# Performance work log

Measured on AMD Instinct MI355X. Metric: run time of the kernel, lower is better.

## Reference

```python
import jax, jax.numpy as jnp
import numpy as np

V, E, CIN, COUT, NH, HID = 8192, 2048, 128, 128, 4, 32
EPS = 1e-5

def _ln(x, g, b):
    m = x.mean(-1, keepdims=True)
    v = x.var(-1, keepdims=True)
    return (x - m) / jnp.sqrt(v + EPS) * g + b

def setup_inputs() -> dict:
    key = jax.random.key(0)
    ks = jax.random.split(key, 12)
    s = 0.05
    X = jax.random.normal(ks[0], (V, CIN), jnp.float32)
    H = jax.random.bernoulli(ks[1], 0.02, (V, E)).astype(jnp.float32)
    edge_features = jax.random.normal(ks[2], (E, COUT), jnp.float32)
    Wv = jax.random.normal(ks[3], (CIN, COUT), jnp.float32) * s
    bv = jnp.zeros((COUT,), jnp.float32)
    We = jax.random.normal(ks[4], (COUT, COUT), jnp.float32) * s
    be = jnp.zeros((COUT,), jnp.float32)
    vW1 = jax.random.normal(ks[5], (NH, CIN, HID), jnp.float32) * s
    vb1 = jnp.zeros((NH, HID), jnp.float32)
    vW2 = jax.random.normal(ks[6], (NH, HID), jnp.float32) * s
    vb2 = jnp.zeros((NH,), jnp.float32)
    eW1 = jax.random.normal(ks[7], (COUT, HID), jnp.float32) * s
    eb1 = jnp.zeros((HID,), jnp.float32)
    eW2 = jax.random.normal(ks[8], (HID,), jnp.float32) * s
    eb2 = jnp.zeros((), jnp.float32)
    Wc = jax.random.normal(ks[9], (NH * COUT, COUT), jnp.float32) * s
    bc = jnp.zeros((COUT,), jnp.float32)
    Wg = jax.random.normal(ks[10], (CIN + COUT, COUT), jnp.float32) * s
    bg = jnp.zeros((COUT,), jnp.float32)
    return dict(X=X, H=H, edge_features=edge_features, Wv=Wv, bv=bv, We=We, be=be,
                vW1=vW1, vb1=vb1, vW2=vW2, vb2=vb2, eW1=eW1, eb1=eb1, eW2=eW2, eb2=eb2,
                Wc=Wc, bc=bc,
                ln_e_g=jnp.ones((COUT,), jnp.float32), ln_e_b=jnp.zeros((COUT,), jnp.float32),
                ln_v_g=jnp.ones((COUT,), jnp.float32), ln_v_b=jnp.zeros((COUT,), jnp.float32),
                bn_g=jnp.ones((COUT,), jnp.float32), bn_b=jnp.zeros((COUT,), jnp.float32),
                Wg=Wg, bg=bg)

def reference(X, H, edge_features, Wv, bv, We, be, vW1, vb1, vW2, vb2,
              eW1, eb1, eW2, eb2, Wc, bc, ln_e_g, ln_e_b, ln_v_g, ln_v_b,
              bn_g, bn_b, Wg, bg):
    gelu = lambda t: jax.nn.gelu(t, approximate=False)  # torch nn.GELU default (erf)
    Ht = H.T                                   # (E, V)
    Xt = X @ Wv + bv                           # (V, Cout) theta_v
    # per-head vertex attention MLP: Linear(Cin,32)->GELU->Linear(32,1), vectorized over heads
    hid = gelu(jnp.einsum('vc,hck->hvk', X, vW1) + vb1[:, None, :])
    attn = jax.nn.sigmoid(jnp.einsum('hvk,hk->hv', hid, vW2) + vb2[:, None])  # (NH, V)
    deg = Ht.sum(axis=1, keepdims=True)        # (E, 1) edge degrees
    denom = jnp.maximum(deg, 1.0)
    # degree-normalized attention-weighted v2e aggregation per head
    head_e = jnp.einsum('ev,hvc->hec', Ht, Xt[None] * attn[:, :, None]) / denom[None]
    e_cat = jnp.transpose(head_e, (1, 0, 2)).reshape(E, NH * COUT)  # concat heads dim=1
    e_feat = e_cat @ Wc + bc                   # attn_combine
    # edge attention uses the LAST head's vertex weights (global-var quirk in torch code)
    edge_att = ((Ht @ attn[-1]) / jnp.maximum(deg[:, 0], 1.0))[:, None]  # (E,1)
    # edge-feature gating with e_attention head 0
    te = edge_features @ We + be               # theta_e
    e_scores = gelu(e_feat @ eW1 + eb1) @ eW2 + eb2
    ew = jax.nn.sigmoid(e_scores)[:, None]
    e_feat = e_feat * ew + te * (1.0 - ew)
    # normalize == 'both': layer_norm_e then batch_norm (training-mode batch stats)
    e_feat = _ln(e_feat, ln_e_g, ln_e_b)
    m = e_feat.mean(axis=0)
    v = e_feat.var(axis=0)
    e_feat = (e_feat - m) / jnp.sqrt(v + EPS) * bn_g + bn_b
    # e2v sum aggregation: H @ e_feat
    v_feat = H @ e_feat                        # (V, Cout)
    gate = jax.nn.sigmoid(jnp.concatenate([X, v_feat], axis=1) @ Wg + bg)
    v_feat = gate * v_feat + (1.0 - gate) * Xt
    v_feat = _ln(v_feat, ln_v_g, ln_v_b)
    v_feat = v_feat + X                        # residual (Cin == Cout)
    v_feat = gelu(v_feat)                      # not is_last: activation; dropout = identity (eval)
    e_feat = gelu(e_feat)
    return v_feat, e_feat, edge_att
```

## Files before the change

kernel.cpp:

```cpp
#include <hip/hip_runtime.h>
#include <hip/hip_bf16.h>
#include <math.h>

#define NV 8192
#define NE 2048
#define CIN 128
#define COUT 128
#define NH 4
#define HID 32
#define EPB 4
#define LCAP 256
#define VCAP 96
#define NWORDS (NE / 64)
#define TWORDS (NV / 64)
#define EPSV 1e-5f

__device__ __forceinline__ float gelu_f(float x) {
    return 0.5f * x * (1.0f + erff(x * 0.70710678118654752f));
}
__device__ __forceinline__ float sigmoid_f(float x) {
    return 1.0f / (1.0f + expf(-x));
}

__global__ __launch_bounds__(256) void k_front(
    const float* __restrict__ X, const float* __restrict__ Wv, const float* __restrict__ bv,
    const float* __restrict__ vW1, const float* __restrict__ vb1,
    const float* __restrict__ vW2, const float* __restrict__ vb2,
    const float* __restrict__ H,
    float* __restrict__ Xt, float* __restrict__ attn4,
    unsigned long long* __restrict__ Hbits, int* __restrict__ vdeg, int* __restrict__ vlist)
{
    __shared__ float Xs[2][8][CIN];
    int t = threadIdx.x;
    if (blockIdx.x < NV / 16) {
        int half = t >> 7, tt = t & 127;
        int v0 = blockIdx.x * 16 + half * 8;
        for (int v = 0; v < 8; ++v) Xs[half][v][tt] = X[(size_t)(v0 + v) * CIN + tt];
        __syncthreads();

        float acc[8];
        float bvc = bv[tt];
#pragma unroll
        for (int v = 0; v < 8; ++v) acc[v] = bvc;
        for (int k = 0; k < CIN; ++k) {
            float w = Wv[k * COUT + tt];
#pragma unroll
            for (int v = 0; v < 8; ++v) acc[v] = fmaf(Xs[half][v][k], w, acc[v]);
        }
        for (int v = 0; v < 8; ++v) Xt[(size_t)(v0 + v) * COUT + tt] = acc[v];

        int h = tt >> 5, j = tt & 31;
        float hb = vb1[h * HID + j];
#pragma unroll
        for (int v = 0; v < 8; ++v) acc[v] = hb;
        for (int k = 0; k < CIN; ++k) {
            float w = vW1[(h * CIN + k) * HID + j];
#pragma unroll
            for (int v = 0; v < 8; ++v) acc[v] = fmaf(Xs[half][v][k], w, acc[v]);
        }
        float w2 = vW2[h * HID + j];
        float b2 = vb2[h];
        for (int v = 0; v < 8; ++v) {
            float val = gelu_f(acc[v]) * w2;
#pragma unroll
            for (int m = 16; m >= 1; m >>= 1) val += __shfl_xor(val, m, 64);
            if (j == 0) attn4[(size_t)(v0 + v) * NH + h] = sigmoid_f(val + b2);
        }
    } else {
        int b = blockIdx.x - NV / 16;
        int w = t >> 6;
        int lane = t & 63;
        int v = b * 4 + w;
        const float* row = H + (size_t)v * NE;
        unsigned long long lt = (1ull << lane) - 1ull;
        int base = 0;
        int* vl = vlist + (size_t)v * VCAP;
#pragma unroll 8
        for (int it = 0; it < NWORDS; ++it) {
            float hv = row[it * 64 + lane];
            bool nz = hv != 0.0f;
            unsigned long long m = __ballot(nz);
            if (lane == 0) Hbits[(size_t)v * NWORDS + it] = m;
            if (nz) {
                int pos = base + __popcll(m & lt);
                if (pos < VCAP) vl[pos] = it * 64 + lane;
            }
            base += __popcll(m);
        }
        if (lane == 0) vdeg[v] = base;
    }
}

__global__ __launch_bounds__(256) void k_transpose(
    const unsigned long long* __restrict__ Hbits, unsigned long long* __restrict__ HbitsT)
{
    __shared__ unsigned long long rows[64][NWORDS];
    int t = threadIdx.x;
    int vt = blockIdx.x;
    for (int i = t; i < 64 * NWORDS; i += 256)
        rows[i >> 5][i & 31] = Hbits[(size_t)vt * 64 * NWORDS + i];
    __syncthreads();
    int wv = t >> 6;
    int lane = t & 63;
    const unsigned long long M[6] = {
        0xFFFFFFFF00000000ULL, 0xFFFF0000FFFF0000ULL, 0xFF00FF00FF00FF00ULL,
        0xF0F0F0F0F0F0F0F0ULL, 0xCCCCCCCCCCCCCCCCULL, 0xAAAAAAAAAAAAAAAAULL };
    const int js[6] = {32, 16, 8, 4, 2, 1};
#pragma unroll
    for (int itb = 0; itb < 8; ++itb) {
        int it = wv * 8 + itb;
        unsigned long long x = rows[lane][it];
#pragma unroll
        for (int s = 0; s < 6; ++s) {
            int j = js[s];
            unsigned long long y = __shfl_xor(x, j, 64);
            unsigned long long Ms = M[s];
            if ((lane & j) == 0) x = (x & ~Ms) | ((y << j) & Ms);
            else                 x = (x & Ms) | ((y >> j) & ~Ms);
        }
        HbitsT[(size_t)(it * 64 + lane) * TWORDS + vt] = x;
    }
}

__global__ __launch_bounds__(512) void k_edge(
    const float* __restrict__ Xt, const float* __restrict__ attn4,
    const unsigned long long* __restrict__ HbitsT,
    const float* __restrict__ edge_features,
    const float* __restrict__ Wc, const float* __restrict__ bc,
    const float* __restrict__ We, const float* __restrict__ be,
    const float* __restrict__ eW1, const float* __restrict__ eb1,
    const float* __restrict__ eW2, const float* __restrict__ eb2,
    const float* __restrict__ ln_g, const float* __restrict__ ln_b,
    float* __restrict__ e_ln, float* __restrict__ out_att,
    float* __restrict__ bn_sum, float* __restrict__ bn_sq)
{
    __shared__ int lst[EPB][LCAP];
    __shared__ int wsum[EPB][2];
    __shared__ float scratch[4096];
    __shared__ float ecat[EPB][NH * COUT];
    __shared__ float efr_s[EPB][COUT];
    __shared__ float efs[EPB][COUT];
    __shared__ float teL[EPB][COUT];
    __shared__ float ews[EPB];
    __shared__ float asp[EPB][2];
    __shared__ float red[EPB][2][2];

    int t = threadIdx.x;
    int g = t >> 7;
    int c = t & 127;
    int lane = t & 63;
    int gw = (t >> 6) & 1;
    int e = blockIdx.x * EPB + g;

    efr_s[g][c] = edge_features[(size_t)e * COUT + c];

    unsigned long long wd = HbitsT[(size_t)e * TWORDS + c];
    int cntT = __popcll(wd);
    int inc = cntT;
#pragma unroll
    for (int s = 1; s < 64; s <<= 1) {
        int y = __shfl_up(inc, s, 64);
        if (lane >= s) inc += y;
    }
    if (lane == 63) wsum[g][gw] = inc;
    __syncthreads();
    int base = (gw ? wsum[g][0] : 0) + inc - cntT;
    int n0 = wsum[g][0] + wsum[g][1];
    int vbase = c * 64;
    unsigned long long mm = wd;
    while (mm) {
        int i = __ffsll(mm) - 1;
        mm &= mm - 1;
        if (base < LCAP) lst[g][base] = vbase + i;
        ++base;
    }
    __syncthreads();

    float inv = 1.0f / fmaxf((float)n0, 1.0f);
    int n = n0 < LCAP ? n0 : LCAP;

    float p00 = 0, p10 = 0, p20 = 0, p30 = 0;
    float p01 = 0, p11 = 0, p21 = 0, p31 = 0;
    float as = 0;
    for (int i = gw; i < n; i += 2) {
        int v = lst[g][i];
        float x0 = Xt[(size_t)v * COUT + lane];
        float x1 = Xt[(size_t)v * COUT + lane + 64];
        float4 a = *(const float4*)(attn4 + (size_t)v * NH);
        p00 = fmaf(x0, a.x, p00);  p01 = fmaf(x1, a.x, p01);
        p10 = fmaf(x0, a.y, p10);  p11 = fmaf(x1, a.y, p11);
        p20 = fmaf(x0, a.z, p20);  p21 = fmaf(x1, a.z, p21);
        p30 = fmaf(x0, a.w, p30);  p31 = fmaf(x1, a.w, p31);
        as += a.w;
    }
    {
        int bi = (g * 2 + gw) * NH * COUT;
        scratch[bi + 0 * COUT + lane] = p00;  scratch[bi + 0 * COUT + lane + 64] = p01;
        scratch[bi + 1 * COUT + lane] = p10;  scratch[bi + 1 * COUT + lane + 64] = p11;
        scratch[bi + 2 * COUT + lane] = p20;  scratch[bi + 2 * COUT + lane + 64] = p21;
        scratch[bi + 3 * COUT + lane] = p30;  scratch[bi + 3 * COUT + lane + 64] = p31;
    }
    if (lane == 0) asp[g][gw] = as;
    __syncthreads();

#pragma unroll
    for (int h = 0; h < NH; ++h)
        ecat[g][h * COUT + c] =
            (scratch[(g * 2 + 0) * NH * COUT + h * COUT + c] +
             scratch[(g * 2 + 1) * NH * COUT + h * COUT + c]) * inv;
    if (c == 0) out_att[e] = (asp[g][0] + asp[g][1]) * inv;
    __syncthreads();

    {
        float accW[EPB] = {0, 0, 0, 0};
        const float* wp = Wc + (size_t)(g * 128) * COUT + c;
        for (int k = 0; k < 128; ++k) {
            float w = wp[k * COUT];
#pragma unroll
            for (int ee = 0; ee < EPB; ++ee)
                accW[ee] = fmaf(ecat[ee][g * 128 + k], w, accW[ee]);
        }
#pragma unroll
        for (int ee = 0; ee < EPB; ++ee) scratch[g * 512 + ee * COUT + c] = accW[ee];

        float accT[EPB] = {0, 0, 0, 0};
        const float* wt = We + (size_t)(g * 32) * COUT + c;
        for (int k = 0; k < 32; ++k) {
            float w = wt[k * COUT];
#pragma unroll
            for (int ee = 0; ee < EPB; ++ee)
                accT[ee] = fmaf(efr_s[ee][g * 32 + k], w, accT[ee]);
        }
#pragma unroll
        for (int ee = 0; ee < EPB; ++ee) scratch[2048 + g * 512 + ee * COUT + c] = accT[ee];
    }
    __syncthreads();

    efs[g][c] = scratch[0 * 512 + g * COUT + c] + scratch[1 * 512 + g * COUT + c]
              + scratch[2 * 512 + g * COUT + c] + scratch[3 * 512 + g * COUT + c] + bc[c];
    teL[g][c] = scratch[2048 + 0 * 512 + g * COUT + c] + scratch[2048 + 1 * 512 + g * COUT + c]
              + scratch[2048 + 2 * 512 + g * COUT + c] + scratch[2048 + 3 * 512 + g * COUT + c] + be[c];
    __syncthreads();

    if (t < 128) {
        int ee = t >> 5, j = t & 31;
        float hj = eb1[j];
        for (int k = 0; k < COUT; ++k) hj = fmaf(efs[ee][k], eW1[k * HID + j], hj);
        float val = gelu_f(hj) * eW2[j];
#pragma unroll
        for (int m = 16; m >= 1; m >>= 1) val += __shfl_xor(val, m, 32);
        if ((t & 31) == 0) ews[ee] = sigmoid_f(val + eb2[0]);
    }
    __syncthreads();

    float y;
    {
        float ew = ews[g];
        float x = efs[g][c] * ew + teL[g][c] * (1.0f - ew);
        float s = x, q = x * x;
#pragma unroll
        for (int m = 32; m >= 1; m >>= 1) { s += __shfl_xor(s, m, 64); q += __shfl_xor(q, m, 64); }
        if (lane == 0) { red[g][gw][0] = s; red[g][gw][1] = q; }
        __syncthreads();
        float S = red[g][0][0] + red[g][1][0];
        float Q = red[g][0][1] + red[g][1][1];
        float m = S * (1.0f / COUT);
        float var = Q * (1.0f / COUT) - m * m;
        y = (x - m) * rsqrtf(var + EPSV) * ln_g[c] + ln_b[c];
        e_ln[(size_t)e * COUT + c] = y;
    }
    scratch[g * COUT + c] = y;
    scratch[512 + g * COUT + c] = y * y;
    __syncthreads();
    if (t < 128) {
        float s = scratch[t] + scratch[COUT + t] + scratch[2 * COUT + t] + scratch[3 * COUT + t];
        float q = scratch[512 + t] + scratch[512 + COUT + t] + scratch[512 + 2 * COUT + t] + scratch[512 + 3 * COUT + t];
        atomicAdd(&bn_sum[t], s);
        atomicAdd(&bn_sq[t], q);
    }
}

__global__ __launch_bounds__(256) void k_bnapply(const float* __restrict__ e_ln,
    const float* __restrict__ bn_sum, const float* __restrict__ bn_sq,
    const float* __restrict__ bn_g, const float* __restrict__ bn_b,
    float* __restrict__ out_e)
{
    int idx = blockIdx.x * 256 + threadIdx.x;
    int c = idx & 127;
    float m = bn_sum[c] * (1.0f / NE);
    float var = bn_sq[c] * (1.0f / NE) - m * m;
    float x = e_ln[idx];
    float y = (x - m) * rsqrtf(var + EPSV) * bn_g[c] + bn_b[c];
    out_e[idx] = gelu_f(y);
}

__global__ __launch_bounds__(512) void k_vertex2(
    const float* __restrict__ X, const int* __restrict__ vdeg, const int* __restrict__ vlist,
    const float* __restrict__ e_ln,
    const float* __restrict__ bn_sum, const float* __restrict__ bn_sq,
    const float* __restrict__ bn_g, const float* __restrict__ bn_b,
    const float* __restrict__ Xt,
    const float* __restrict__ Wg, const float* __restrict__ bg,
    const float* __restrict__ ln_g, const float* __restrict__ ln_b,
    float* __restrict__ out_v)
{
    __shared__ float XsF[8 * CIN];
    __shared__ float vfF[8 * COUT];
    __shared__ int lst[8][VCAP];
    __shared__ int degs[8];
    __shared__ float part[4 * 8 * COUT];
    __shared__ float red[8][2][2];

    int t = threadIdx.x;
    int vg = t >> 6, lane = t & 63;
    int g4 = t >> 7, c = t & 127;
    int gw2 = (t >> 6) & 1;
    int v0 = blockIdx.x * 8;

    {
        float2 x2 = *(const float2*)(X + (size_t)(v0 + vg) * CIN + lane * 2);
        XsF[vg * CIN + lane * 2] = x2.x;
        XsF[vg * CIN + lane * 2 + 1] = x2.y;
    }
    for (int i = t; i < 8 * VCAP; i += 512)
        lst[i / VCAP][i % VCAP] = vlist[(size_t)v0 * VCAP + i];
    if (t < 8) degs[t] = vdeg[v0 + t];
    __syncthreads();

    int ch0 = lane * 2;
    float m0 = bn_sum[ch0] * (1.0f / NE);
    float m1 = bn_sum[ch0 + 1] * (1.0f / NE);
    float A0 = bn_g[ch0] * rsqrtf(bn_sq[ch0] * (1.0f / NE) - m0 * m0 + EPSV);
    float A1 = bn_g[ch0 + 1] * rsqrtf(bn_sq[ch0 + 1] * (1.0f / NE) - m1 * m1 + EPSV);
    float B0 = bn_b[ch0] - m0 * A0;
    float B1 = bn_b[ch0 + 1] - m1 * A1;

    int n = degs[vg];
    if (n > VCAP) n = VCAP;
    float sx = 0, sy = 0;
    for (int i = 0; i < n; ++i) {
        float2 v2 = *(const float2*)(e_ln + (size_t)lst[vg][i] * COUT + ch0);
        sx += v2.x;
        sy += v2.y;
    }
    float fn = (float)n;
    vfF[vg * COUT + ch0] = A0 * sx + fn * B0;
    vfF[vg * COUT + ch0 + 1] = A1 * sy + fn * B1;
    __syncthreads();

    {
        float accW[8] = {0, 0, 0, 0, 0, 0, 0, 0};
        const float* wp = Wg + (size_t)(g4 * 64) * COUT + c;
        const float* src = (g4 < 2) ? XsF : vfF;
        int kb = (g4 & 1) * 64;
        for (int ki = 0; ki < 64; ++ki) {
            float w = wp[(size_t)ki * COUT];
#pragma unroll
            for (int v = 0; v < 8; ++v)
                accW[v] = fmaf(src[v * 128 + kb + ki], w, accW[v]);
        }
#pragma unroll
        for (int v = 0; v < 8; ++v) part[g4 * 1024 + v * COUT + c] = accW[v];
    }
    __syncthreads();

    float xv[2];
#pragma unroll
    for (int rep = 0; rep < 2; ++rep) {
        int v = g4 + rep * 4;
        float ag = part[0 * 1024 + v * COUT + c] + part[1 * 1024 + v * COUT + c]
                 + part[2 * 1024 + v * COUT + c] + part[3 * 1024 + v * COUT + c] + bg[c];
        float gate = sigmoid_f(ag);
        float x = gate * vfF[v * COUT + c] + (1.0f - gate) * Xt[(size_t)(v0 + v) * COUT + c];
        xv[rep] = x;
        float s = x, q = x * x;
#pragma unroll
        for (int m = 32; m >= 1; m >>= 1) { s += __shfl_xor(s, m, 64); q += __shfl_xor(q, m, 64); }
        if (lane == 0) { red[v][gw2][0] = s; red[v][gw2][1] = q; }
    }
    __syncthreads();
#pragma unroll
    for (int rep = 0; rep < 2; ++rep) {
        int v = g4 + rep * 4;
        float S = red[v][0][0] + red[v][1][0];
        float Q = red[v][0][1] + red[v][1][1];
        float m_ = S * (1.0f / COUT);
        float var = Q * (1.0f / COUT) - m_ * m_;
        float y = (xv[rep] - m_) * rsqrtf(var + EPSV) * ln_g[c] + ln_b[c];
        y = y + XsF[v * CIN + c];
        out_v[(size_t)(v0 + v) * COUT + c] = gelu_f(y);
    }
}

extern "C" void kernel_launch(void* const* d_in, const int* in_sizes, int n_in,
                              void* d_out, int out_size, void* d_ws, size_t ws_size,
                              hipStream_t stream) {
    const float* X    = (const float*)d_in[0];
    const float* H    = (const float*)d_in[1];
    const float* edge_features = (const float*)d_in[2];
    const float* Wv   = (const float*)d_in[3];
    const float* bv   = (const float*)d_in[4];
    const float* We   = (const float*)d_in[5];
    const float* be   = (const float*)d_in[6];
    const float* vW1  = (const float*)d_in[7];
    const float* vb1  = (const float*)d_in[8];
    const float* vW2  = (const float*)d_in[9];
    const float* vb2  = (const float*)d_in[10];
    const float* eW1  = (const float*)d_in[11];
    const float* eb1  = (const float*)d_in[12];
    const float* eW2  = (const float*)d_in[13];
    const float* eb2  = (const float*)d_in[14];
    const float* Wc   = (const float*)d_in[15];
    const float* bc   = (const float*)d_in[16];
    const float* ln_e_g = (const float*)d_in[17];
    const float* ln_e_b = (const float*)d_in[18];
    const float* ln_v_g = (const float*)d_in[19];
    const float* ln_v_b = (const float*)d_in[20];
    const float* bn_g = (const float*)d_in[21];
    const float* bn_b = (const float*)d_in[22];
    const float* Wg   = (const float*)d_in[23];
    const float* bg   = (const float*)d_in[24];

    float* out_v  = (float*)d_out;
    float* out_e  = out_v + NV * COUT;
    float* out_att = out_e + NE * COUT;

    char* w = (char*)d_ws;
    float* Xt     = (float*)w; w += (size_t)NV * COUT * 4;
    float* attn4  = (float*)w; w += (size_t)NV * NH * 4;
    float* e_ln   = (float*)w; w += (size_t)NE * COUT * 4;
    float* bn_sum = (float*)w; w += COUT * 4;
    float* bn_sq  = (float*)w; w += COUT * 4;
    int*   vdeg   = (int*)w;   w += (size_t)NV * 4;
    int*   vlist  = (int*)w;   w += (size_t)NV * VCAP * 4;
    unsigned long long* Hbits  = (unsigned long long*)w; w += (size_t)NV * NWORDS * 8;
    unsigned long long* HbitsT = (unsigned long long*)w; w += (size_t)NE * TWORDS * 8;

    hipMemsetAsync(bn_sum, 0, 2 * COUT * sizeof(float), stream);

    k_front<<<NV / 16 + NV / 4, 256, 0, stream>>>(X, Wv, bv, vW1, vb1, vW2, vb2, H,
                                                  Xt, attn4, Hbits, vdeg, vlist);
    k_transpose<<<NV / 64, 256, 0, stream>>>(Hbits, HbitsT);
    k_edge<<<NE / EPB, 512, 0, stream>>>(Xt, attn4, HbitsT, edge_features,
                                         Wc, bc, We, be, eW1, eb1, eW2, eb2,
                                         ln_e_g, ln_e_b, e_ln, out_att, bn_sum, bn_sq);
    k_bnapply<<<(NE * COUT) / 256, 256, 0, stream>>>(e_ln, bn_sum, bn_sq, bn_g, bn_b, out_e);
    k_vertex2<<<NV / 8, 512, 0, stream>>>(X, vdeg, vlist, e_ln, bn_sum, bn_sq, bn_g, bn_b,
                                          Xt, Wg, bg, ln_v_g, ln_v_b, out_v);
}
```

Measured before the change: 263.6 us.

## Vectorize incidence-row scan and spread edge gather over four waves per edge

The H-row scan in k_front now reads float4s, with 16 edges per lane, and builds 64-bit masks through shuffles instead of one ballot per 64 floats, which cuts load instructions on the dense 64MB incidence matrix. k_edge drops from 4 to 2 edges per 512-thread block, so four waves instead of two gather the incident-vertex features for each edge, giving more memory parallelism on the irregular gather. The side cost is twice as many blocks, more per-edge global atomics for the batch-norm sums, and a __syncthreads inside divergent branches. That barrier relies on both branches reaching a matching barrier, which is fragile.

After: 268.7 us. No clear change (+1.9%).

```diff
diff --git a/kernel.cpp b/kernel.cpp
--- a/kernel.cpp
+++ b/kernel.cpp
@@ -8,7 +8,7 @@
 #define COUT 128
 #define NH 4
 #define HID 32
-#define EPB 4
+#define EPB 2
 #define LCAP 256
 #define VCAP 96
 #define NWORDS (NE / 64)
@@ -71,21 +71,55 @@
         int w = t >> 6;
         int lane = t & 63;
         int v = b * 4 + w;
-        const float* row = H + (size_t)v * NE;
-        unsigned long long lt = (1ull << lane) - 1ull;
+        const float4* row4 = (const float4*)(H + (size_t)v * NE);
         int base = 0;
         int* vl = vlist + (size_t)v * VCAP;
-#pragma unroll 8
-        for (int it = 0; it < NWORDS; ++it) {
-            float hv = row[it * 64 + lane];
-            bool nz = hv != 0.0f;
-            unsigned long long m = __ballot(nz);
-            if (lane == 0) Hbits[(size_t)v * NWORDS + it] = m;
-            if (nz) {
-                int pos = base + __popcll(m & lt);
-                if (pos < VCAP) vl[pos] = it * 64 + lane;
+#pragma unroll
+        for (int it = 0; it < NE / 1024; ++it) {
+            int e0 = it * 1024 + lane * 16;
+            float4 f0 = row4[it * 256 + lane * 4 + 0];
+            float4 f1 = row4[it * 256 + lane * 4 + 1];
+            float4 f2 = row4[it * 256 + lane * 4 + 2];
+            float4 f3 = row4[it * 256 + lane * 4 + 3];
+            unsigned int m16 = 0;
+            m16 |= (f0.x != 0.0f ? 1u : 0u) << 0;  m16 |= (f0.y != 0.0f ? 1u : 0u) << 1;
+            m16 |= (f0.z != 0.0f ? 1u : 0u) << 2;  m16 |= (f0.w != 0.0f ? 1u : 0u) << 3;
+            m16 |= (f1.x != 0.0f ? 1u : 0u) << 4;  m16 |= (f1.y != 0.0f ? 1u : 0u) << 5;
+            m16 |= (f1.z != 0.0f ? 1u : 0u) << 6;  m16 |= (f1.w != 0.0f ? 1u : 0u) << 7;
+            m16 |= (f2.x != 0.0f ? 1u : 0u) << 8;  m16 |= (f2.y != 0.0f ? 1u : 0u) << 9;
+            m16 |= (f2.z != 0.0f ? 1u : 0u) << 10; m16 |= (f2.w != 0.0f ? 1u : 0u) << 11;
+            m16 |= (f3.x != 0.0f ? 1u : 0u) << 12; m16 |= (f3.y != 0.0f ? 1u : 0u) << 13;
+            m16 |= (f3.z != 0.0f ? 1u : 0u) << 14; m16 |= (f3.w != 0.0f ? 1u : 0u) << 15;
+
+            int cnt = __popc(m16);
+            int inc = cnt;
+#pragma unroll
+            for (int s = 1; s < 64; s <<= 1) {
+                int y = __shfl_up(inc, s, 64);
+                if (lane >= s) inc += y;
             }
-            base += __popcll(m);
+            int tot = __shfl(inc, 63, 64);
+            int q = lane & 15;
+            unsigned int w0 = __shfl(m16, q * 4 + 0, 64);
+            unsigned int w1 = __shfl(m16, q * 4 + 1, 64);
+            unsigned int w2 = __shfl(m16, q * 4 + 2, 64);
+            unsigned int w3 = __shfl(m16, q * 4 + 3, 64);
+            if (lane < 16) {
+                unsigned long long word = (unsigned long long)w0
+                    | ((unsigned long long)w1 << 16)
+                    | ((unsigned long long)w2 << 32)
+                    | ((unsigned long long)w3 << 48);
+                Hbits[(size_t)v * NWORDS + it * 16 + lane] = word;
+            }
+            int off = base + inc - cnt;
+            unsigned int mm = m16;
+            while (mm) {
+                int j = __ffs(mm) - 1;
+                mm &= mm - 1;
+                if (off < VCAP) vl[off] = e0 + j;
+                ++off;
+            }
+            base += tot;
         }
         if (lane == 0) vdeg[v] = base;
     }
@@ -136,53 +170,59 @@
 {
     __shared__ int lst[EPB][LCAP];
     __shared__ int wsum[EPB][2];
-    __shared__ float scratch[4096];
+    __shared__ float sc[4096];
     __shared__ float ecat[EPB][NH * COUT];
     __shared__ float efr_s[EPB][COUT];
     __shared__ float efs[EPB][COUT];
     __shared__ float teL[EPB][COUT];
     __shared__ float ews[EPB];
-    __shared__ float asp[EPB][2];
+    __shared__ float asp[EPB][4];
     __shared__ float red[EPB][2][2];
 
     int t = threadIdx.x;
-    int g = t >> 7;
-    int c = t & 127;
+    int g = t >> 8;
+    int tg = t & 255;
+    int wv = tg >> 6;
     int lane = t & 63;
-    int gw = (t >> 6) & 1;
     int e = blockIdx.x * EPB + g;
 
-    efr_s[g][c] = edge_features[(size_t)e * COUT + c];
-
-    unsigned long long wd = HbitsT[(size_t)e * TWORDS + c];
-    int cntT = __popcll(wd);
-    int inc = cntT;
-#pragma unroll
-    for (int s = 1; s < 64; s <<= 1) {
-        int y = __shfl_up(inc, s, 64);
-        if (lane >= s) inc += y;
-    }
-    if (lane == 63) wsum[g][gw] = inc;
-    __syncthreads();
-    int base = (gw ? wsum[g][0] : 0) + inc - cntT;
+    if (tg < 128) efr_s[g][tg] = edge_features[(size_t)e * COUT + tg];
+
+    if (tg < 128) {
+        int gw = tg >> 6;
+        unsigned long long wd = HbitsT[(size_t)e * TWORDS + tg];
+        int cntT = __popcll(wd);
+        int inc = cntT;
+#pragma unroll
+        for (int s = 1; s < 64; s <<= 1) {
+            int y = __shfl_up(inc, s, 64);
+            if (lane >= s) inc += y;
+        }
+        if (lane == 63) wsum[g][gw] = inc;
+        __syncthreads();
+        int base = (gw ? wsum[g][0] : 0) + inc - cntT;
+        int vbase = tg * 64;
+        unsigned long long mm = wd;
+        while (mm) {
+            int i = __ffsll(mm) - 1;
+            mm &= mm - 1;
+            if (base < LCAP) lst[g][base] = vbase + i;
+            ++base;
+        }
+    } else {
+        __syncthreads();
+    }
+    __syncthreads();
+
     int n0 = wsum[g][0] + wsum[g][1];
-    int vbase = c * 64;
-    unsigned long long mm = wd;
-    while (mm) {
-        int i = __ffsll(mm) - 1;
-        mm &= mm - 1;
-        if (base < LCAP) lst[g][base] = vbase + i;
-        ++base;
-    }
-    __syncthreads();
-
     float inv = 1.0f / fmaxf((float)n0, 1.0f);
     int n = n0 < LCAP ? n0 : LCAP;
 
     float p00 = 0, p10 = 0, p20 = 0, p30 = 0;
     float p01 = 0, p11 = 0, p21 = 0, p31 = 0;
     float as = 0;
-    for (int i = gw; i < n; i += 2) {
+#pragma unroll 2
+    for (int i = wv; i < n; i += 4) {
         int v = lst[g][i];
         float x0 = Xt[(size_t)v * COUT + lane];
         float x1 = Xt[(size_t)v * COUT + lane + 64];
@@ -194,55 +234,61 @@
         as += a.w;
     }
     {
-        int bi = (g * 2 + gw) * NH * COUT;
-        scratch[bi + 0 * COUT + lane] = p00;  scratch[bi + 0 * COUT + lane + 64] = p01;
-        scratch[bi + 1 * COUT + lane] = p10;  scratch[bi + 1 * COUT + lane + 64] = p11;
-        scratch[bi + 2 * COUT + lane] = p20;  scratch[bi + 2 * COUT + lane + 64] = p21;
-        scratch[bi + 3 * COUT + lane] = p30;  scratch[bi + 3 * COUT + lane + 64] = p31;
-    }
-    if (lane == 0) asp[g][gw] = as;
-    __syncthreads();
-
-#pragma unroll
-    for (int h = 0; h < NH; ++h)
-        ecat[g][h * COUT + c] =
-            (scratch[(g * 2 + 0) * NH * COUT + h * COUT + c] +
-             scratch[(g * 2 + 1) * NH * COUT + h * COUT + c]) * inv;
-    if (c == 0) out_att[e] = (asp[g][0] + asp[g][1]) * inv;
+        int bi = g * 2048 + wv * 512;
+        sc[bi + 0 * COUT + lane] = p00;  sc[bi + 0 * COUT + lane + 64] = p01;
+        sc[bi + 1 * COUT + lane] = p10;  sc[bi + 1 * COUT + lane + 64] = p11;
+        sc[bi + 2 * COUT + lane] = p20;  sc[bi + 2 * COUT + lane + 64] = p21;
+        sc[bi + 3 * COUT + lane] = p30;  sc[bi + 3 * COUT + lane + 64] = p31;
+    }
+    if (lane == 0) asp[g][wv] = as;
+    __syncthreads();
+
+#pragma unroll
+    for (int r = 0; r < 2; ++r) {
+        int k = tg + r * 256;
+        int bi = g * 2048 + k;
+        ecat[g][k] = (sc[bi] + sc[bi + 512] + sc[bi + 1024] + sc[bi + 1536]) * inv;
+    }
+    if (tg == 0) out_att[e] = (asp[g][0] + asp[g][1] + asp[g][2] + asp[g][3]) * inv;
     __syncthreads();
 
     {
-        float accW[EPB] = {0, 0, 0, 0};
-        const float* wp = Wc + (size_t)(g * 128) * COUT + c;
+        int g4 = t >> 7, c = t & 127;
+        float accW[EPB] = {0, 0};
+        const float* wp = Wc + (size_t)(g4 * 128) * COUT + c;
         for (int k = 0; k < 128; ++k) {
             float w = wp[k * COUT];
 #pragma unroll
             for (int ee = 0; ee < EPB; ++ee)
-                accW[ee] = fmaf(ecat[ee][g * 128 + k], w, accW[ee]);
-        }
-#pragma unroll
-        for (int ee = 0; ee < EPB; ++ee) scratch[g * 512 + ee * COUT + c] = accW[ee];
-
-        float accT[EPB] = {0, 0, 0, 0};
-        const float* wt = We + (size_t)(g * 32) * COUT + c;
+                accW[ee] = fmaf(ecat[ee][g4 * 128 + k], w, accW[ee]);
+        }
+        float accT[EPB] = {0, 0};
+        const float* wt = We + (size_t)(g4 * 32) * COUT + c;
         for (int k = 0; k < 32; ++k) {
             float w = wt[k * COUT];
 #pragma unroll
             for (int ee = 0; ee < EPB; ++ee)
-                accT[ee] = fmaf(efr_s[ee][g * 32 + k], w, accT[ee]);
-        }
-#pragma unroll
-        for (int ee = 0; ee < EPB; ++ee) scratch[2048 + g * 512 + ee * COUT + c] = accT[ee];
-    }
-    __syncthreads();
-
-    efs[g][c] = scratch[0 * 512 + g * COUT + c] + scratch[1 * 512 + g * COUT + c]
-              + scratch[2 * 512 + g * COUT + c] + scratch[3 * 512 + g * COUT + c] + bc[c];
-    teL[g][c] = scratch[2048 + 0 * 512 + g * COUT + c] + scratch[2048 + 1 * 512 + g * COUT + c]
-              + scratch[2048 + 2 * 512 + g * COUT + c] + scratch[2048 + 3 * 512 + g * COUT + c] + be[c];
-    __syncthreads();
-
-    if (t < 128) {
+                accT[ee] = fmaf(efr_s[ee][g4 * 32 + k], w, accT[ee]);
+        }
+        __syncthreads();
+#pragma unroll
+        for (int ee = 0; ee < EPB; ++ee) {
+            sc[g4 * 256 + ee * 128 + c] = accW[ee];
+            sc[1024 + g4 * 256 + ee * 128 + c] = accT[ee];
+        }
+    }
+    __syncthreads();
+
+    if (t < 256) {
+        int ee = t >> 7, c = t & 127;
+        efs[ee][c] = sc[0 * 256 + ee * 128 + c] + sc[1 * 256 + ee * 128 + c]
+                   + sc[2 * 256 + ee * 128 + c] + sc[3 * 256 + ee * 128 + c] + bc[c];
+        teL[ee][c] = sc[1024 + 0 * 256 + ee * 128 + c] + sc[1024 + 1 * 256 + ee * 128 + c]
+                   + sc[1024 + 2 * 256 + ee * 128 + c] + sc[1024 + 3 * 256 + ee * 128 + c] + be[c];
+    }
+    __syncthreads();
+
+    if (t < 64) {
         int ee = t >> 5, j = t & 31;
         float hj = eb1[j];
         for (int k = 0; k < COUT; ++k) hj = fmaf(efs[ee][k], eW1[k * HID + j], hj);
@@ -253,28 +299,31 @@
     }
     __syncthreads();
 
-    float y;
-    {
+    float xb = 0;
+    if (tg < 128) {
+        int gw = tg >> 6;
         float ew = ews[g];
-        float x = efs[g][c] * ew + teL[g][c] * (1.0f - ew);
-        float s = x, q = x * x;
+        xb = efs[g][tg] * ew + teL[g][tg] * (1.0f - ew);
+        float s = xb, q = xb * xb;
 #pragma unroll
         for (int m = 32; m >= 1; m >>= 1) { s += __shfl_xor(s, m, 64); q += __shfl_xor(q, m, 64); }
         if (lane == 0) { red[g][gw][0] = s; red[g][gw][1] = q; }
-        __syncthreads();
+    }
+    __syncthreads();
+    if (tg < 128) {
         float S = red[g][0][0] + red[g][1][0];
         float Q = red[g][0][1] + red[g][1][1];
         float m = S * (1.0f / COUT);
         float var = Q * (1.0f / COUT) - m * m;
-        y = (x - m) * rsqrtf(var + EPSV) * ln_g[c] + ln_b[c];
-        e_ln[(size_t)e * COUT + c] = y;
-    }
-    scratch[g * COUT + c] = y;
-    scratch[512 + g * COUT + c] = y * y;
+        float y = (xb - m) * rsqrtf(var + EPSV) * ln_g[tg] + ln_b[tg];
+        e_ln[(size_t)e * COUT + tg] = y;
+        sc[g * 128 + tg] = y;
+        sc[256 + g * 128 + tg] = y * y;
+    }
     __syncthreads();
     if (t < 128) {
-        float s = scratch[t] + scratch[COUT + t] + scratch[2 * COUT + t] + scratch[3 * COUT + t];
-        float q = scratch[512 + t] + scratch[512 + COUT + t] + scratch[512 + 2 * COUT + t] + scratch[512 + 3 * COUT + t];
+        float s = sc[t] + sc[128 + t];
+        float q = sc[256 + t] + sc[384 + t];
         atomicAdd(&bn_sum[t], s);
         atomicAdd(&bn_sq[t], q);
     }
```
